# Performance work log

Measured on AMD Instinct MI355X. Metric: run time of the kernel, lower is better.

## Reference

```python
import jax, jax.numpy as jnp
import numpy as np

B, C, S, H = 64, 64, 128, 512   # batch, num_centroid, max_seq_length, hidden_size
D = S * H
EPS = 1e-8


def setup_inputs() -> dict:
    key = jax.random.key(0)
    k1, k2 = jax.random.split(key)
    return {
        "input": jax.random.normal(k1, (B, D), dtype=jnp.float32),
        "centroid_weight": jax.random.normal(k2, (C, D), dtype=jnp.float32),
    }


def _gram(x):
    # x: (..., S, H) -> (..., S, S)
    return jnp.einsum('...sh,...th->...st', x, x)


def _centering(g):
    # H @ g @ H with H = I - 11^T/n  ==  g - rowmean - colmean + grandmean
    rm = jnp.mean(g, axis=-1, keepdims=True)
    cm = jnp.mean(g, axis=-2, keepdims=True)
    gm = jnp.mean(g, axis=(-1, -2), keepdims=True)
    return g - rm - cm + gm


def reference(input, centroid_weight):
    # torch.cdist(input, centroid_weight), p=2
    x2 = jnp.sum(input * input, axis=1, keepdims=True)        # (B,1)
    w2 = jnp.sum(centroid_weight * centroid_weight, axis=1)   # (C,)
    d2 = x2 + w2[None, :] - 2.0 * (input @ centroid_weight.T)
    dist = jnp.sqrt(jnp.maximum(d2, 0.0))                     # (B,C)

    xb = input.reshape(B, S, H)
    cw = centroid_weight.reshape(C, S, H)

    cgx = _centering(_gram(xb))   # (B,S,S)
    cgy = _centering(_gram(cw))   # (C,S,S)

    # linear HSIC(x,y) summed over last two dims, broadcast (B,1)x(C) -> (B,C)
    hxy = jnp.einsum('bst,cst->bc', cgx, cgy)
    hxx = jnp.sum(cgx * cgx, axis=(-1, -2))   # (B,)
    hyy = jnp.sum(cgy * cgy, axis=(-1, -2))   # (C,)
    cka_mat = -jnp.log(
        jnp.abs(hxy / (jnp.sqrt(hxx)[:, None] * jnp.sqrt(hyy)[None, :])) + EPS
    )  # (B,C)

    idx = jnp.argmax(cka_mat, axis=-1)                 # (B,)
    sel = centroid_weight[idx].reshape(B, S, H)        # selected centroids
    cgs = _centering(_gram(sel))                       # (B,S,S)

    # second CKA: x is (B,1,S,S), y is (B,S,S) -> broadcast to (B,B) as in torch
    hxy2 = jnp.einsum('bst,cst->bc', cgx, cgs)         # (B,B)
    hyy2 = jnp.sum(cgs * cgs, axis=(-1, -2))           # (B,)
    ratio = jnp.abs(hxy2 / (jnp.sqrt(hxx)[:, None] * jnp.sqrt(hyy2)[None, :]))
    cka_loss = -jnp.log(jnp.mean(ratio) + EPS)         # scalar

    return (cka_loss, dist, centroid_weight, idx)
```

## Files before the change

kernel.cpp:

```cpp
#include <hip/hip_runtime.h>
#include <math.h>

#define Bn 64
#define Cn 64
#define Sn 128
#define Hn 512
#define Dn 65536
#define SSn 16384

using f32x4 = __attribute__((ext_vector_type(4))) float;
using bf16x8 = __attribute__((ext_vector_type(8))) short;

__device__ __forceinline__ float wredf(float v) {
#pragma unroll
    for (int o = 32; o > 0; o >>= 1) v += __shfl_down(v, o, 64);
    return v;
}

__device__ __forceinline__ unsigned short f2bf(float f) {
    unsigned int u = __float_as_uint(f);
    u += 0x7fffu + ((u >> 16) & 1u);
    return (unsigned short)(u >> 16);
}
__device__ __forceinline__ float bf2f(unsigned short h) {
    return __uint_as_float(((unsigned int)h) << 16);
}

__global__ __launch_bounds__(512) void kA(const float* __restrict__ x,
                                          const float* __restrict__ w,
                                          float* __restrict__ gF,
                                          float* __restrict__ rsT,
                                          float* __restrict__ hpartG,
                                          float* __restrict__ x2,
                                          float* __restrict__ w2,
                                          float* __restrict__ partials,
                                          float* __restrict__ outcpy) {
    __shared__ __align__(16) unsigned char smem[67584];
    const int bid = blockIdx.x;
    const int tid = threadIdx.x;
    if (bid >= 256) {
        const int cid = bid - 256;
        const float4* wsrc = (const float4*)w;
#pragma unroll 4
        for (int p = 0; p < 32; ++p) {
            const size_t f4i = (size_t)cid * 16384 + tid + 512 * p;
            float4 v = wsrc[f4i];
            float* dst = outcpy + 4 * f4i;
            dst[0] = v.x; dst[1] = v.y; dst[2] = v.z; dst[3] = v.w;
        }
        return;
    }
    const int lane = tid & 63;
    const int wv = tid >> 6;
    const int lrow = lane & 15;
    const int lk8 = (lane >> 4) * 8;
    const int crow4 = (lane >> 4) * 4;
    if (bid < 128) {
        __shared__ float sA[8], sB[8];
        const int mat = bid;
        const float* src = (mat < Bn) ? (x + (size_t)mat * Dn) : (w + (size_t)(mat - Bn) * Dn);
        unsigned short (*hi)[72] = (unsigned short(*)[72])smem;
        unsigned short (*lo)[72] = (unsigned short(*)[72])(smem + 18432);
        f32x4 acc[8] = {};
        float ssq = 0.f;
        float4 cur[4], nxt[4];
#pragma unroll
        for (int p = 0; p < 4; ++p) {
            const int f = tid + 512 * p;
            cur[p] = *(const float4*)(src + (size_t)(f >> 4) * Hn + (f & 15) * 4);
        }
        for (int c = 0; c < 8; ++c) {
#pragma unroll
            for (int p = 0; p < 4; ++p) {
                const int f = tid + 512 * p;
                const int r = f >> 4, c4 = (f & 15) * 4;
                float4 v = cur[p];
                ssq += v.x * v.x + v.y * v.y + v.z * v.z + v.w * v.w;
                unsigned short h0 = f2bf(v.x), h1 = f2bf(v.y), h2 = f2bf(v.z), h3 = f2bf(v.w);
                *(ushort4*)&hi[r][c4] = make_ushort4(h0, h1, h2, h3);
                *(ushort4*)&lo[r][c4] = make_ushort4(f2bf(v.x - bf2f(h0)), f2bf(v.y - bf2f(h1)),
                                                     f2bf(v.z - bf2f(h2)), f2bf(v.w - bf2f(h3)));
            }
            if (c < 7) {
#pragma unroll
                for (int p = 0; p < 4; ++p) {
                    const int f = tid + 512 * p;
                    nxt[p] = *(const float4*)(src + (size_t)(f >> 4) * Hn + (c + 1) * 64 + (f & 15) * 4);
                }
            }
            __syncthreads();
#pragma unroll
            for (int ks = 0; ks < 64; ks += 32) {
                const int arow = wv * 16 + lrow;
                bf16x8 ah = *(const bf16x8*)&hi[arow][ks + lk8];
                bf16x8 al = *(const bf16x8*)&lo[arow][ks + lk8];
#pragma unroll
                for (int j = 0; j < 8; ++j) {
                    const int brow = j * 16 + lrow;
                    bf16x8 bh = *(const bf16x8*)&hi[brow][ks + lk8];
                    bf16x8 bl = *(const bf16x8*)&lo[brow][ks + lk8];
                    acc[j] = __builtin_amdgcn_mfma_f32_16x16x32_bf16(ah, bh, acc[j], 0, 0, 0);
                    acc[j] = __builtin_amdgcn_mfma_f32_16x16x32_bf16(ah, bl, acc[j], 0, 0, 0);
                    acc[j] = __builtin_amdgcn_mfma_f32_16x16x32_bf16(al, bh, acc[j], 0, 0, 0);
                }
            }
            __syncthreads();
            if (c < 7) {
#pragma unroll
                for (int p = 0; p < 4; ++p) cur[p] = nxt[p];
            }
        }
        float* dst = gF + (size_t)mat * SSn + wv * 2048;
        float sq = 0.f;
#pragma unroll
        for (int j = 0; j < 8; ++j) {
            f32x4 v = acc[j];
            sq += v[0] * v[0] + v[1] * v[1] + v[2] * v[2] + v[3] * v[3];
            *(f32x4*)(dst + j * 256 + lane * 4) = v;
        }
#pragma unroll
        for (int r = 0; r < 4; ++r) {
            float rs = 0.f;
#pragma unroll
            for (int j = 0; j < 8; ++j) rs += acc[j][r];
            rs += __shfl_xor(rs, 1, 64);
            rs += __shfl_xor(rs, 2, 64);
            rs += __shfl_xor(rs, 4, 64);
            rs += __shfl_xor(rs, 8, 64);
            if (lrow == 0) rsT[(size_t)(wv * 16 + crow4 + r) * 128 + mat] = rs;
        }
        sq = wredf(sq);
        ssq = wredf(ssq);
        if (lane == 0) { sA[wv] = sq; sB[wv] = ssq; }
        __syncthreads();
        if (tid == 0) {
            float g2 = 0.f, tr = 0.f;
#pragma unroll
            for (int i = 0; i < 8; ++i) { g2 += sA[i]; tr += sB[i]; }
            hpartG[mat] = g2;
            if (mat < Bn) x2[mat] = tr; else w2[mat - Bn] = tr;
        }
    } else {
        const int did = bid - 128;
        unsigned short (*la)[264] = (unsigned short(*)[264])smem;
        unsigned short (*lb)[264] = (unsigned short(*)[264])(smem + 33792);
        const int rg = wv >> 1, cgb = (wv & 1) * 2;
        f32x4 acc[2] = {};
        for (int cc = 0; cc < 2; ++cc) {
            const int k0 = did * 512 + cc * 256;
            __syncthreads();
#pragma unroll
            for (int p = 0; p < 8; ++p) {
                const int f = tid + 512 * p;
                const int row = f >> 6, c4 = (f & 63) * 4;
                float4 vx = *(const float4*)(x + (size_t)row * Dn + k0 + c4);
                float4 vw = *(const float4*)(w + (size_t)row * Dn + k0 + c4);
                *(ushort4*)&la[row][c4] = make_ushort4(f2bf(vx.x), f2bf(vx.y), f2bf(vx.z), f2bf(vx.w));
                *(ushort4*)&lb[row][c4] = make_ushort4(f2bf(vw.x), f2bf(vw.y), f2bf(vw.z), f2bf(vw.w));
            }
            __syncthreads();
#pragma unroll
            for (int ks = 0; ks < 8; ++ks) {
                bf16x8 a = *(const bf16x8*)&la[rg * 16 + lrow][ks * 32 + lk8];
#pragma unroll
                for (int q = 0; q < 2; ++q) {
                    bf16x8 b = *(const bf16x8*)&lb[(cgb + q) * 16 + lrow][ks * 32 + lk8];
                    acc[q] = __builtin_amdgcn_mfma_f32_16x16x32_bf16(a, b, acc[q], 0, 0, 0);
                }
            }
        }
        float* p = partials + (size_t)did * 4096;
#pragma unroll
        for (int q = 0; q < 2; ++q)
#pragma unroll
            for (int r = 0; r < 4; ++r)
                p[(rg * 16 + crow4 + r) * 64 + (cgb + q) * 16 + lrow] = acc[q][r];
    }
}

__global__ __launch_bounds__(256) void kB(const float* __restrict__ gF,
                                          const float* __restrict__ partials,
                                          const float* __restrict__ rsT,
                                          const float* __restrict__ hpartG,
                                          const float* __restrict__ x2,
                                          const float* __restrict__ w2,
                                          float* __restrict__ partials2,
                                          float* __restrict__ Sv,
                                          float* __restrict__ hxx,
                                          float* __restrict__ hyy,
                                          float* __restrict__ od) {
    __shared__ __align__(16) unsigned char smem[65536];
    const int bid = blockIdx.x;
    const int tid = threadIdx.x;
    if (bid < 256) {
        float (*la)[68] = (float(*)[68])smem;
        float (*lb)[68] = (float(*)[68])(smem + 17408);
        const int k0 = bid * 64;
        const int slc = (tid & 15) * 4;
        for (int r = tid >> 4; r < 64; r += 16) {
            *(float4*)&la[r][slc] = *(const float4*)(gF + (size_t)r * SSn + k0 + slc);
            *(float4*)&lb[r][slc] = *(const float4*)(gF + (size_t)(64 + r) * SSn + k0 + slc);
        }
        __syncthreads();
        const int ry = tid >> 4, tx = tid & 15;
        float acc[4][4] = {};
        for (int k = 0; k < 64; k += 4) {
            float4 av[4], bv[4];
#pragma unroll
            for (int i = 0; i < 4; ++i) av[i] = *(const float4*)&la[4 * ry + i][k];
#pragma unroll
            for (int j = 0; j < 4; ++j) bv[j] = *(const float4*)&lb[16 * j + tx][k];
#pragma unroll
            for (int i = 0; i < 4; ++i)
#pragma unroll
                for (int j = 0; j < 4; ++j)
                    acc[i][j] += av[i].x * bv[j].x + av[i].y * bv[j].y +
                                 av[i].z * bv[j].z + av[i].w * bv[j].w;
        }
        float* p = partials2 + (size_t)bid * 4096;
#pragma unroll
        for (int i = 0; i < 4; ++i)
#pragma unroll
            for (int j = 0; j < 4; ++j)
                p[(4 * ry + i) * 64 + 16 * j + tx] = acc[i][j];
    } else if (bid < 320) {
        double* red = (double*)smem;
        const int b2 = bid - 256;
        const int o = tid & 63, sl = tid >> 6;
        const int i = b2 * 64 + o;
        double s = 0;
        for (int t = 0; t < 32; ++t)
            s += (double)partials[(size_t)(sl + 4 * t) * 4096 + i];
        red[sl * 64 + o] = s;
        __syncthreads();
        if (tid < 64) {
            double t = red[tid] + red[64 + tid] + red[128 + tid] + red[192 + tid];
            float d2 = x2[b2] + w2[tid] - 2.f * (float)t;
            od[b2 * 64 + tid] = sqrtf(fmaxf(d2, 0.f));
        }
    } else {
        float* rl = (float*)smem;
        for (int p = 0; p < 16; ++p) {
            const int f4 = tid + 256 * p;
            *(float4*)(rl + 4 * f4) = *(const float4*)(rsT + 4 * f4);
        }
        __syncthreads();
        if (tid < 128) {
            float s = 0.f, q = 0.f;
            for (int t = 0; t < 128; ++t) {
                float v = rl[t * 128 + tid];
                s += v; q += v * v;
            }
            Sv[tid] = s;
            double val = (double)hpartG[tid] - (double)q * (1.0 / 64.0)
                       + (double)s * (double)s * (1.0 / 16384.0);
            if (tid < 64) hxx[tid] = (float)val; else hyy[tid - 64] = (float)val;
        }
    }
}

__global__ __launch_bounds__(256) void kC(const float* __restrict__ partials2,
                                          const float* __restrict__ rsT,
                                          const float* __restrict__ Sv,
                                          double* __restrict__ hxy) {
    __shared__ double red[256];
    const int b = blockIdx.x;
    const int o = threadIdx.x & 63;
    const int sl = threadIdx.x >> 6;
    const int i = b * 64 + o;
    double s0 = 0, s1 = 0;
    for (int t = 0; t < 64; t += 2) {
        s0 += (double)partials2[(size_t)(sl + 4 * t) * 4096 + i];
        s1 += (double)partials2[(size_t)(sl + 4 * (t + 1)) * 4096 + i];
    }
    double corr = 0;
    for (int t = 0; t < 32; ++t) {
        const int ss = sl * 32 + t;
        corr += (double)rsT[ss * 128 + b] * (double)rsT[ss * 128 + 64 + o];
    }
    red[sl * 64 + o] = (s0 + s1) - corr * (1.0 / 64.0);
    __syncthreads();
    if (threadIdx.x < 64) {
        double t = red[threadIdx.x] + red[64 + threadIdx.x] +
                   red[128 + threadIdx.x] + red[192 + threadIdx.x];
        t += (double)Sv[b] * (double)Sv[64 + threadIdx.x] * (1.0 / 16384.0);
        hxy[b * 64 + threadIdx.x] = t;
    }
}

__global__ void finalize_k(const double* __restrict__ hxy, const float* __restrict__ hxx,
                           const float* __restrict__ hyy, float* __restrict__ out0,
                           float* __restrict__ oidx) {
    __shared__ double inv_sx[64], inv_sy[64];
    __shared__ double qv[256];
    __shared__ int qi[256];
    __shared__ int sidx[64];
    __shared__ double sred[4];
    const int tid = threadIdx.x;
    if (tid < 64) {
        inv_sx[tid] = 1.0 / sqrt((double)hxx[tid]);
        inv_sy[tid] = 1.0 / sqrt((double)hyy[tid]);
    }
    __syncthreads();
    {
        const int b = tid >> 2, q = tid & 3;
        double best = 1e300; int bi = 64;
        for (int c = q * 16; c < q * 16 + 16; ++c) {
            double v = fabs(hxy[b * 64 + c]) * inv_sy[c];
            if (v < best) { best = v; bi = c; }
        }
        qv[tid] = best; qi[tid] = bi;
    }
    __syncthreads();
    if (tid < 64) {
        double best = qv[4 * tid]; int bi = qi[4 * tid];
        for (int q = 1; q < 4; ++q) {
            if (qv[4 * tid + q] < best) { best = qv[4 * tid + q]; bi = qi[4 * tid + q]; }
        }
        sidx[tid] = bi;
        oidx[tid] = (float)bi;
    }
    __syncthreads();
    double s = 0.0;
    for (int e = tid; e < 4096; e += 256) {
        const int b = e >> 6, c = e & 63;
        const int ic = sidx[c];
        s += fabs(hxy[b * 64 + ic]) * inv_sx[b] * inv_sy[ic];
    }
#pragma unroll
    for (int o = 32; o > 0; o >>= 1) s += __shfl_down(s, o, 64);
    if ((tid & 63) == 0) sred[tid >> 6] = s;
    __syncthreads();
    if (tid == 0) {
        double t = sred[0] + sred[1] + sred[2] + sred[3];
        out0[0] = (float)(-log(t / 4096.0 + 1e-8));
    }
}

extern "C" void kernel_launch(void* const* d_in, const int* in_sizes, int n_in,
                              void* d_out, int out_size, void* d_ws, size_t ws_size,
                              hipStream_t stream) {
    const float* x = (const float*)d_in[0];
    const float* w = (const float*)d_in[1];
    float* out = (float*)d_out;
    float* ws = (float*)d_ws;
    float* gF        = ws;
    float* partials  = ws + 2097152;
    float* partials2 = ws + 2621440;
    float* rsT       = ws + 3670016;
    float* hpartG    = ws + 3686400;
    float* Sv        = ws + 3686528;
    float* x2        = ws + 3686656;
    float* w2        = ws + 3686720;
    float* hxx       = ws + 3686784;
    float* hyy       = ws + 3686848;
    double* hxyD     = (double*)(ws + 3686912);

    kA<<<320, 512, 0, stream>>>(x, w, gF, rsT, hpartG, x2, w2, partials, out + 4097);
    kB<<<321, 256, 0, stream>>>(gF, partials, rsT, hpartG, x2, w2,
                                partials2, Sv, hxx, hyy, out + 1);
    kC<<<64, 256, 0, stream>>>(partials2, rsT, Sv, hxyD);
    finalize_k<<<1, 256, 0, stream>>>(hxyD, hxx, hyy, out, out + 4198401);
}
```

Measured before the change: 113.0 us.

## Fuse centroid copy into distance blocks, retile Gram MFMA warps, reduce split-K

Removes the dedicated copy blocks and writes the centroid output from the distance-GEMM blocks that already load it. Retiles the Gram MFMA so each warp computes a 32x64 tile, improving LDS operand reuse, with row sums combined through shared memory. Cuts the cross-Gram split-K from 256 to 64 blocks looping over 4 chunks, shrinking the partials written and summed in kC. Trades fewer launched blocks and less parallelism for less memory traffic and reduction work.

```diff
diff --git a/kernel.cpp b/kernel.cpp
--- a/kernel.cpp
+++ b/kernel.cpp
@@ -38,18 +38,6 @@
     __shared__ __align__(16) unsigned char smem[67584];
     const int bid = blockIdx.x;
     const int tid = threadIdx.x;
-    if (bid >= 256) {
-        const int cid = bid - 256;
-        const float4* wsrc = (const float4*)w;
-#pragma unroll 4
-        for (int p = 0; p < 32; ++p) {
-            const size_t f4i = (size_t)cid * 16384 + tid + 512 * p;
-            float4 v = wsrc[f4i];
-            float* dst = outcpy + 4 * f4i;
-            dst[0] = v.x; dst[1] = v.y; dst[2] = v.z; dst[3] = v.w;
-        }
-        return;
-    }
     const int lane = tid & 63;
     const int wv = tid >> 6;
     const int lrow = lane & 15;
@@ -58,10 +46,12 @@
     if (bid < 128) {
         __shared__ float sA[8], sB[8];
         const int mat = bid;
+        const int wm = wv >> 1;
+        const int wc = wv & 1;
         const float* src = (mat < Bn) ? (x + (size_t)mat * Dn) : (w + (size_t)(mat - Bn) * Dn);
         unsigned short (*hi)[72] = (unsigned short(*)[72])smem;
         unsigned short (*lo)[72] = (unsigned short(*)[72])(smem + 18432);
-        f32x4 acc[8] = {};
+        f32x4 acc[2][4] = {};
         float ssq = 0.f;
         float4 cur[4], nxt[4];
 #pragma unroll
@@ -91,17 +81,24 @@
             __syncthreads();
 #pragma unroll
             for (int ks = 0; ks < 64; ks += 32) {
-                const int arow = wv * 16 + lrow;
-                bf16x8 ah = *(const bf16x8*)&hi[arow][ks + lk8];
-                bf16x8 al = *(const bf16x8*)&lo[arow][ks + lk8];
-#pragma unroll
-                for (int j = 0; j < 8; ++j) {
-                    const int brow = j * 16 + lrow;
+                bf16x8 ah[2], al[2];
+#pragma unroll
+                for (int i = 0; i < 2; ++i) {
+                    const int arow = wm * 32 + i * 16 + lrow;
+                    ah[i] = *(const bf16x8*)&hi[arow][ks + lk8];
+                    al[i] = *(const bf16x8*)&lo[arow][ks + lk8];
+                }
+#pragma unroll
+                for (int j = 0; j < 4; ++j) {
+                    const int brow = wc * 64 + j * 16 + lrow;
                     bf16x8 bh = *(const bf16x8*)&hi[brow][ks + lk8];
                     bf16x8 bl = *(const bf16x8*)&lo[brow][ks + lk8];
-                    acc[j] = __builtin_amdgcn_mfma_f32_16x16x32_bf16(ah, bh, acc[j], 0, 0, 0);
-                    acc[j] = __builtin_amdgcn_mfma_f32_16x16x32_bf16(ah, bl, acc[j], 0, 0, 0);
-                    acc[j] = __builtin_amdgcn_mfma_f32_16x16x32_bf16(al, bh, acc[j], 0, 0, 0);
+#pragma unroll
+                    for (int i = 0; i < 2; ++i) {
+                        acc[i][j] = __builtin_amdgcn_mfma_f32_16x16x32_bf16(ah[i], bh, acc[i][j], 0, 0, 0);
+                        acc[i][j] = __builtin_amdgcn_mfma_f32_16x16x32_bf16(ah[i], bl, acc[i][j], 0, 0, 0);
+                        acc[i][j] = __builtin_amdgcn_mfma_f32_16x16x32_bf16(al[i], bh, acc[i][j], 0, 0, 0);
+                    }
                 }
             }
             __syncthreads();
@@ -113,26 +110,30 @@
         float* dst = gF + (size_t)mat * SSn + wv * 2048;
         float sq = 0.f;
 #pragma unroll
-        for (int j = 0; j < 8; ++j) {
-            f32x4 v = acc[j];
-            sq += v[0] * v[0] + v[1] * v[1] + v[2] * v[2] + v[3] * v[3];
-            *(f32x4*)(dst + j * 256 + lane * 4) = v;
-        }
-#pragma unroll
-        for (int r = 0; r < 4; ++r) {
-            float rs = 0.f;
-#pragma unroll
-            for (int j = 0; j < 8; ++j) rs += acc[j][r];
-            rs += __shfl_xor(rs, 1, 64);
-            rs += __shfl_xor(rs, 2, 64);
-            rs += __shfl_xor(rs, 4, 64);
-            rs += __shfl_xor(rs, 8, 64);
-            if (lrow == 0) rsT[(size_t)(wv * 16 + crow4 + r) * 128 + mat] = rs;
-        }
+        for (int i = 0; i < 2; ++i)
+#pragma unroll
+            for (int j = 0; j < 4; ++j) {
+                f32x4 v = acc[i][j];
+                sq += v[0] * v[0] + v[1] * v[1] + v[2] * v[2] + v[3] * v[3];
+                *(f32x4*)(dst + (i * 4 + j) * 256 + lane * 4) = v;
+            }
+        float* sRS = (float*)smem;
+#pragma unroll
+        for (int i = 0; i < 2; ++i)
+#pragma unroll
+            for (int r = 0; r < 4; ++r) {
+                float rs = acc[i][0][r] + acc[i][1][r] + acc[i][2][r] + acc[i][3][r];
+                rs += __shfl_xor(rs, 1, 64);
+                rs += __shfl_xor(rs, 2, 64);
+                rs += __shfl_xor(rs, 4, 64);
+                rs += __shfl_xor(rs, 8, 64);
+                if (lrow == 0) sRS[(wm * 32 + i * 16 + crow4 + r) * 2 + wc] = rs;
+            }
         sq = wredf(sq);
         ssq = wredf(ssq);
         if (lane == 0) { sA[wv] = sq; sB[wv] = ssq; }
         __syncthreads();
+        if (tid < 128) rsT[(size_t)tid * 128 + mat] = sRS[tid * 2] + sRS[tid * 2 + 1];
         if (tid == 0) {
             float g2 = 0.f, tr = 0.f;
 #pragma unroll
@@ -157,6 +158,8 @@
                 float4 vw = *(const float4*)(w + (size_t)row * Dn + k0 + c4);
                 *(ushort4*)&la[row][c4] = make_ushort4(f2bf(vx.x), f2bf(vx.y), f2bf(vx.z), f2bf(vx.w));
                 *(ushort4*)&lb[row][c4] = make_ushort4(f2bf(vw.x), f2bf(vw.y), f2bf(vw.z), f2bf(vw.w));
+                float* dc = outcpy + (size_t)row * Dn + k0 + c4;
+                dc[0] = vw.x; dc[1] = vw.y; dc[2] = vw.z; dc[3] = vw.w;
             }
             __syncthreads();
 #pragma unroll
@@ -192,30 +195,33 @@
     __shared__ __align__(16) unsigned char smem[65536];
     const int bid = blockIdx.x;
     const int tid = threadIdx.x;
-    if (bid < 256) {
+    if (bid < 64) {
         float (*la)[68] = (float(*)[68])smem;
         float (*lb)[68] = (float(*)[68])(smem + 17408);
-        const int k0 = bid * 64;
         const int slc = (tid & 15) * 4;
-        for (int r = tid >> 4; r < 64; r += 16) {
-            *(float4*)&la[r][slc] = *(const float4*)(gF + (size_t)r * SSn + k0 + slc);
-            *(float4*)&lb[r][slc] = *(const float4*)(gF + (size_t)(64 + r) * SSn + k0 + slc);
-        }
-        __syncthreads();
         const int ry = tid >> 4, tx = tid & 15;
         float acc[4][4] = {};
-        for (int k = 0; k < 64; k += 4) {
-            float4 av[4], bv[4];
-#pragma unroll
-            for (int i = 0; i < 4; ++i) av[i] = *(const float4*)&la[4 * ry + i][k];
-#pragma unroll
-            for (int j = 0; j < 4; ++j) bv[j] = *(const float4*)&lb[16 * j + tx][k];
-#pragma unroll
-            for (int i = 0; i < 4; ++i)
-#pragma unroll
-                for (int j = 0; j < 4; ++j)
-                    acc[i][j] += av[i].x * bv[j].x + av[i].y * bv[j].y +
-                                 av[i].z * bv[j].z + av[i].w * bv[j].w;
+        for (int c = 0; c < 4; ++c) {
+            const int k0 = bid * 256 + c * 64;
+            __syncthreads();
+            for (int r = tid >> 4; r < 64; r += 16) {
+                *(float4*)&la[r][slc] = *(const float4*)(gF + (size_t)r * SSn + k0 + slc);
+                *(float4*)&lb[r][slc] = *(const float4*)(gF + (size_t)(64 + r) * SSn + k0 + slc);
+            }
+            __syncthreads();
+            for (int k = 0; k < 64; k += 4) {
+                float4 av[4], bv[4];
+#pragma unroll
+                for (int i = 0; i < 4; ++i) av[i] = *(const float4*)&la[4 * ry + i][k];
+#pragma unroll
+                for (int j = 0; j < 4; ++j) bv[j] = *(const float4*)&lb[16 * j + tx][k];
+#pragma unroll
+                for (int i = 0; i < 4; ++i)
+#pragma unroll
+                    for (int j = 0; j < 4; ++j)
+                        acc[i][j] += av[i].x * bv[j].x + av[i].y * bv[j].y +
+                                     av[i].z * bv[j].z + av[i].w * bv[j].w;
+            }
         }
         float* p = partials2 + (size_t)bid * 4096;
 #pragma unroll
@@ -223,9 +229,9 @@
 #pragma unroll
             for (int j = 0; j < 4; ++j)
                 p[(4 * ry + i) * 64 + 16 * j + tx] = acc[i][j];
-    } else if (bid < 320) {
+    } else if (bid < 128) {
         double* red = (double*)smem;
-        const int b2 = bid - 256;
+        const int b2 = bid - 64;
         const int o = tid & 63, sl = tid >> 6;
         const int i = b2 * 64 + o;
         double s = 0;
@@ -268,17 +274,15 @@
     const int o = threadIdx.x & 63;
     const int sl = threadIdx.x >> 6;
     const int i = b * 64 + o;
-    double s0 = 0, s1 = 0;
-    for (int t = 0; t < 64; t += 2) {
-        s0 += (double)partials2[(size_t)(sl + 4 * t) * 4096 + i];
-        s1 += (double)partials2[(size_t)(sl + 4 * (t + 1)) * 4096 + i];
-    }
+    double s = 0;
+    for (int t = 0; t < 16; ++t)
+        s += (double)partials2[(size_t)(sl + 4 * t) * 4096 + i];
     double corr = 0;
     for (int t = 0; t < 32; ++t) {
         const int ss = sl * 32 + t;
         corr += (double)rsT[ss * 128 + b] * (double)rsT[ss * 128 + 64 + o];
     }
-    red[sl * 64 + o] = (s0 + s1) - corr * (1.0 / 64.0);
+    red[sl * 64 + o] = s - corr * (1.0 / 64.0);
     __syncthreads();
     if (threadIdx.x < 64) {
         double t = red[threadIdx.x] + red[64 + threadIdx.x] +
@@ -347,17 +351,17 @@
     float* gF        = ws;
     float* partials  = ws + 2097152;
     float* partials2 = ws + 2621440;
-    float* rsT       = ws + 3670016;
-    float* hpartG    = ws + 3686400;
-    float* Sv        = ws + 3686528;
-    float* x2        = ws + 3686656;
-    float* w2        = ws + 3686720;
-    float* hxx       = ws + 3686784;
-    float* hyy       = ws + 3686848;
-    double* hxyD     = (double*)(ws + 3686912);
-
-    kA<<<320, 512, 0, stream>>>(x, w, gF, rsT, hpartG, x2, w2, partials, out + 4097);
-    kB<<<321, 256, 0, stream>>>(gF, partials, rsT, hpartG, x2, w2,
+    float* rsT       = ws + 2883584;
+    float* hpartG    = ws + 2899968;
+    float* Sv        = ws + 2900096;
+    float* x2        = ws + 2900224;
+    float* w2        = ws + 2900288;
+    float* hxx       = ws + 2900352;
+    float* hyy       = ws + 2900416;
+    double* hxyD     = (double*)(ws + 2900480);
+
+    kA<<<256, 512, 0, stream>>>(x, w, gF, rsT, hpartG, x2, w2, partials, out + 4097);
+    kB<<<129, 256, 0, stream>>>(gF, partials, rsT, hpartG, x2, w2,
                                 partials2, Sv, hxx, hyy, out + 1);
     kC<<<64, 256, 0, stream>>>(partials2, rsT, Sv, hxyD);
     finalize_k<<<1, 256, 0, stream>>>(hxyD, hxx, hyy, out, out + 4198401);
```

After: 117.3 us. +3.8%, slower.
